# Kernel optimization log

Hardware: AMD Instinct MI355X
Metric: run time of the kernel (lower is better)

Reference implementation:

```python
import jax, jax.numpy as jnp
import numpy as np

B, D, K = 32, 400, 200
H = 8            # kernel_size (GRU hidden)
LAYERS = 4
OUT = 8


def setup_inputs() -> dict:
    key = jax.random.key(0)
    ks = jax.random.split(key, 16)
    x = jax.random.normal(ks[0], (B, D, K), dtype=jnp.float32)
    # variable-length zero padding along time per (b, k) sequence
    lengths = jax.random.randint(ks[1], (B, K), D // 2, D + 1)
    tmask = jnp.arange(D)[None, :, None] < lengths[:, None, :]   # (B, D, K)
    x = x * tmask
    s = 1.0 / np.sqrt(H)
    def u(k, shape):
        return jax.random.uniform(k, shape, jnp.float32, -s, s)
    return {
        "x": x,
        "w_ih0": u(ks[2], (2, 3 * H, 1)),
        "w_hh0": u(ks[3], (2, 3 * H, H)),
        "b_ih0": u(ks[4], (2, 3 * H)),
        "b_hh0": u(ks[5], (2, 3 * H)),
        "w_ih": u(ks[6], (LAYERS - 1, 2, 3 * H, 2 * H)),
        "w_hh": u(ks[7], (LAYERS - 1, 2, 3 * H, H)),
        "b_ih": u(ks[8], (LAYERS - 1, 2, 3 * H)),
        "b_hh": u(ks[9], (LAYERS - 1, 2, 3 * H)),
        "lin1_w": u(ks[10], (H, 2 * H)),
        "lin1_b": u(ks[11], (H,)),
        "lin2_w": u(ks[12], (OUT, H)),
        "lin2_b": u(ks[13], (OUT,)),
    }


def _gru_dir(x, mask, Wih, Whh, bih, bhh):
    # x: (N, T, in), mask: (N, T) bool -> (N, T, H); zero past each length
    gi = jnp.einsum('nti,gi->tng', x, Wih) + bih          # (T, N, 3H) input gates
    m = mask.T[:, :, None]                                 # (T, N, 1)
    h0 = jnp.zeros((x.shape[0], Whh.shape[1]), x.dtype)
    def step(h, inp):
        gi_t, m_t = inp
        gh = h @ Whh.T + bhh
        ir, iz, inn = jnp.split(gi_t, 3, axis=-1)          # PyTorch gate order r, z, n
        hr, hz, hn = jnp.split(gh, 3, axis=-1)
        r = jax.nn.sigmoid(ir + hr)
        z = jax.nn.sigmoid(iz + hz)
        n = jnp.tanh(inn + r * hn)
        h = jnp.where(m_t, (1.0 - z) * n + z * h, h)
        return h, jnp.where(m_t, h, 0.0)
    _, out = jax.lax.scan(step, h0, (gi, m))
    return out.transpose(1, 0, 2)


def _bidir_gru(x, mask, rev_idx, p):
    Wih, Whh, bih, bhh = p
    fwd = _gru_dir(x, mask, Wih[0], Whh[0], bih[0], bhh[0])
    # backward dir of a packed sequence: reverse within each valid region
    x_rev = jnp.take_along_axis(x, rev_idx[:, :, None], axis=1)
    bwd_rev = _gru_dir(x_rev, mask, Wih[1], Whh[1], bih[1], bhh[1])
    bwd = jnp.take_along_axis(bwd_rev, rev_idx[:, :, None], axis=1)
    bwd = jnp.where(mask[:, :, None], bwd, 0.0)
    return jnp.concatenate([fwd, bwd], axis=-1)


def _forward(x, w_ih0, w_hh0, b_ih0, b_hh0, w_ih, w_hh, b_ih, b_hh,
             lin1_w, lin1_b, lin2_w, lin2_b):
    b, d, k = x.shape
    seq = x.transpose(0, 2, 1).reshape(b * k, d, 1)         # (N, T, 1)
    vals = seq[:, :, 0]
    zm = vals == 0.0
    lengths = jnp.where(zm.any(axis=1), jnp.argmax(zm, axis=1), d)  # (N,)
    mask = jnp.arange(d)[None, :] < lengths[:, None]        # (N, T)
    rev_idx = jnp.clip(lengths[:, None] - 1 - jnp.arange(d)[None, :], 0, d - 1)
    h = _bidir_gru(seq, mask, rev_idx, (w_ih0, w_hh0, b_ih0, b_hh0))
    for l in range(w_ih.shape[0]):                          # layers 1..3
        h = _bidir_gru(h, mask, rev_idx, (w_ih[l], w_hh[l], b_ih[l], b_hh[l]))
    # last valid timestep per sequence (matches argmax-of-all-zero gather)
    last = jnp.take_along_axis(h, (lengths - 1)[:, None, None], axis=1)[:, 0, :]
    feat = last.reshape(b, k, -1)                           # (B, K, 2H)
    y = jax.nn.leaky_relu(feat @ lin1_w.T + lin1_b, negative_slope=0.2)
    return y @ lin2_w.T + lin2_b                            # (B, K, OUT)


def reference(x, w_ih0, w_hh0, b_ih0, b_hh0, w_ih, w_hh, b_ih, b_hh,
              lin1_w, lin1_b, lin2_w, lin2_b):
    return _forward(x, w_ih0, w_hh0, b_ih0, b_hh0, w_ih, w_hh, b_ih, b_hh,
                    lin1_w, lin1_b, lin2_w, lin2_b)
```

## Files before the change

kernel.cpp:

```cpp
#include <hip/hip_runtime.h>

#define BB 32
#define DD 400
#define KK 200
#define NN (BB*KK)
#define NBINS 512

typedef float f2 __attribute__((ext_vector_type(2)));
typedef _Float16 half_t;
typedef _Float16 f16x2 __attribute__((ext_vector_type(2)));

#if defined(__has_builtin)
#if __has_builtin(__builtin_amdgcn_fdot2)
#define HAVE_FDOT2 1
#endif
#endif

__device__ __forceinline__ float dot2(f16x2 w, f16x2 v, float acc) {
#ifdef HAVE_FDOT2
  return __builtin_amdgcn_fdot2(w, v, acc, false);
#else
  return fmaf((float)w.x, (float)v.x, fmaf((float)w.y, (float)v.y, acc));
#endif
}

__device__ __forceinline__ float fast_sigmoid(float x) {
  float e = __builtin_amdgcn_exp2f(-1.4426950408889634f * x);
  return __builtin_amdgcn_rcpf(1.0f + e);
}
__device__ __forceinline__ float fast_tanh(float x) {
  float e = __builtin_amdgcn_exp2f(-2.8853900817779268f * x);
  return 2.0f * __builtin_amdgcn_rcpf(1.0f + e) - 1.0f;
}

#define QPERM(v, P) __int_as_float(__builtin_amdgcn_mov_dpp(__float_as_int(v), (P)*0x55, 0xF, 0xF, true))
#define SWZ_XOR4(v) __int_as_float(__builtin_amdgcn_ds_swizzle(__float_as_int(v), 0x101F))

__global__ __launch_bounds__(256) void transpose_x(const float* __restrict__ x,
                                                   float* __restrict__ xt) {
  __shared__ float tile[32][33];
  int b = blockIdx.x, t0 = blockIdx.y * 32, k0 = blockIdx.z * 32;
  int tx = threadIdx.x, ty = threadIdx.y;
#pragma unroll
  for (int i = 0; i < 32; i += 8) {
    int t = t0 + ty + i, k = k0 + tx;
    tile[ty + i][tx] = (t < DD && k < KK) ? x[((size_t)b * DD + t) * KK + k] : 0.0f;
  }
  __syncthreads();
#pragma unroll
  for (int i = 0; i < 32; i += 8) {
    int k = k0 + ty + i, t = t0 + tx;
    if (k < KK && t < DD) xt[((size_t)b * KK + k) * DD + t] = tile[tx][ty + i];
  }
}

__global__ __launch_bounds__(64) void compute_lengths(const float* __restrict__ xt,
                                                      int* __restrict__ lengths,
                                                      int* __restrict__ hist) {
  int n = blockIdx.x, lane = threadIdx.x;
  int m = DD;
  for (int t = lane; t < DD; t += 64) {
    if (xt[(size_t)n * DD + t] == 0.0f) { m = t; break; }
  }
#pragma unroll
  for (int off = 1; off < 64; off <<= 1) {
    int o = __shfl_xor(m, off, 64);
    m = (o < m) ? o : m;
  }
  if (lane == 0) {
    lengths[n] = m;
    atomicAdd(&hist[m], 1);
  }
}

__global__ __launch_bounds__(64) void scan_offsets(const int* __restrict__ hist,
                                                   int* __restrict__ offs) {
  int lane = threadIdx.x;
  int v[8], tot = 0;
#pragma unroll
  for (int i = 0; i < 8; ++i) { v[i] = tot; tot += hist[lane * 8 + i]; }
  int incl = tot;
#pragma unroll
  for (int off = 1; off < 64; off <<= 1) {
    int oth = __shfl_up(incl, off, 64);
    if (lane >= off) incl += oth;
  }
  int excl = incl - tot;
#pragma unroll
  for (int i = 0; i < 8; ++i) offs[lane * 8 + i] = excl + v[i];
}

__global__ __launch_bounds__(256) void scatter_sort(const int* __restrict__ lengths,
                                                    int* __restrict__ offs,
                                                    int* __restrict__ order,
                                                    int* __restrict__ len_sorted) {
  int n = blockIdx.x * 256 + threadIdx.x;
  if (n >= NN) return;
  int len = lengths[n];
  int pos = atomicAdd(&offs[len], 1);
  order[pos] = n;
  len_sorted[pos] = len;
}

template <int IN_DIM, bool IND_IN, bool WRITE_SEQ, bool FWD_ONLY>
__global__ __launch_bounds__(256) void gru_scan(
    const void* __restrict__ in, half_t* __restrict__ out, float* __restrict__ feat,
    const int* __restrict__ len_sorted, const int* __restrict__ order,
    const float* __restrict__ Wih, const float* __restrict__ Whh,
    const float* __restrict__ bih, const float* __restrict__ bhh, int nseq) {
  int p = (blockIdx.x * 256 + threadIdx.x) >> 6;
  int lane = threadIdx.x & 63;
  int G = FWD_ONLY ? nseq : nseq * 2;
  int W = (G + 7) >> 3;
  if (p >= W) return;
  int o = (p & 1) ? (W - 1 - (p >> 1)) : (p >> 1);
  int gidx = o * 8 + (lane >> 3);
  int li = lane & 7;
  if (gidx >= G) return;
  int sg  = FWD_ONLY ? gidx : (gidx >> 1);
  int dir = FWD_ONLY ? 0 : (gidx & 1);
  int len = len_sorted[sg];

  int qb = li & 4, qbx = qb ^ 4;
  f2 wAB[3][4];
  f16x2 wi2[3][8];
  float wi1[3];
  float bs[3], bh2;
#pragma unroll
  for (int gt = 0; gt < 3; ++gt) {
    int row = dir * 24 + gt * 8 + li;
    if constexpr (IN_DIM == 16) {
#pragma unroll
      for (int q = 0; q < 8; ++q) {
        f16x2 w;
        w.x = (half_t)Wih[row * 16 + 2 * q];
        w.y = (half_t)Wih[row * 16 + 2 * q + 1];
        wi2[gt][q] = w;
      }
    } else {
      wi1[gt] = Wih[row];
    }
#pragma unroll
    for (int P = 0; P < 4; ++P) {
      f2 w; w.x = Whh[row * 8 + qb + P]; w.y = Whh[row * 8 + qbx + P];
      wAB[gt][P] = w;
    }
    bs[gt] = bih[row] + ((gt < 2) ? bhh[row] : 0.0f);
    if (gt == 2) bh2 = bhh[row];
  }

  int steps = len;
  float h = 0.0f, hx = 0.0f;

  const float* px = nullptr;
  const half_t* pxh = nullptr;
  ptrdiff_t xstep;
  if constexpr (IN_DIM == 1) {
    const float* basep = (const float*)in + (IND_IN ? (size_t)order[sg] * DD : (size_t)sg * DD);
    px = basep + ((dir == 0) ? 0 : (len - 1));
    xstep = (dir == 0) ? 1 : -1;
  } else {
    const half_t* basep = (const half_t*)in + (size_t)sg * DD * 16;
    pxh = basep + (size_t)((dir == 0) ? 0 : (len - 1)) * 16;
    xstep = (dir == 0) ? 16 : -16;
  }

  half_t* pw = nullptr; ptrdiff_t wstep = 0;
  if constexpr (WRITE_SEQ) {
    pw = out + ((size_t)sg * DD + ((dir == 0) ? 0 : (len - 1))) * 16 + dir * 8 + li;
    wstep = (dir == 0) ? 16 : -16;
  }

  auto core = [&](float a0, float a1, float a2) {
    float hq0 = QPERM(h, 0), hq1 = QPERM(h, 1), hq2 = QPERM(h, 2), hq3 = QPERM(h, 3);
    float hx0 = QPERM(hx, 0), hx1 = QPERM(hx, 1), hx2 = QPERM(hx, 2), hx3 = QPERM(hx, 3);
    f2 u0; u0.x = hq0; u0.y = hx0;
    f2 u1; u1.x = hq1; u1.y = hx1;
    f2 u2; u2.x = hq2; u2.y = hx2;
    f2 u3; u3.x = hq3; u3.y = hx3;

    f2 c0 = wAB[0][0] * u0; c0 += wAB[0][1] * u1; c0 += wAB[0][2] * u2; c0 += wAB[0][3] * u3;
    f2 c1 = wAB[1][0] * u0; c1 += wAB[1][1] * u1; c1 += wAB[1][2] * u2; c1 += wAB[1][3] * u3;
    f2 c2; c2.x = bh2; c2.y = 0.0f;
    c2 += wAB[2][0] * u0; c2 += wAB[2][1] * u1; c2 += wAB[2][2] * u2; c2 += wAB[2][3] * u3;

    float r = fast_sigmoid(a0 + c0.x + c0.y);
    float z = fast_sigmoid(a1 + c1.x + c1.y);
    float n = fast_tanh(a2 + r * (c2.x + c2.y));
    h = z * (h - n) + n;
    hx = SWZ_XOR4(h);
    if constexpr (WRITE_SEQ) { *pw = (half_t)h; pw += wstep; }
  };

  if constexpr (IN_DIM == 1) {
    float s0_, s1_, s2_, s3_;
    auto ld = [&](float& S_) { S_ = *px; px += xstep; };
    auto st = [&](float& S_, bool pf) {
      float a0 = fmaf(wi1[0], S_, bs[0]);
      float a1 = fmaf(wi1[1], S_, bs[1]);
      float a2 = fmaf(wi1[2], S_, bs[2]);
      if (pf) ld(S_);
      core(a0, a1, a2);
    };
    ld(s0_); ld(s1_); ld(s2_); ld(s3_);
    int t = 0;
    for (; t + 4 <= steps; t += 4) {
      st(s0_, true); st(s1_, true); st(s2_, true); st(s3_, true);
    }
    int rem = steps - t;
    if (rem > 0) st(s0_, false);
    if (rem > 1) st(s1_, false);
    if (rem > 2) st(s2_, false);
  } else {
    uint4 b0_[2], b1_[2], b2_[2], b3_[2];
    auto ld = [&](uint4 (&B_)[2]) {
      const uint4* q4 = reinterpret_cast<const uint4*>(pxh);
      B_[0] = q4[0]; B_[1] = q4[1];
      pxh += xstep;
    };
    auto st = [&](uint4 (&B_)[2], bool pf) {
      float a0 = bs[0], a1 = bs[1], a2 = bs[2];
#pragma unroll
      for (int q = 0; q < 2; ++q) {
        f16x2 p0 = __builtin_bit_cast(f16x2, B_[q].x);
        f16x2 p1 = __builtin_bit_cast(f16x2, B_[q].y);
        f16x2 p2 = __builtin_bit_cast(f16x2, B_[q].z);
        f16x2 p3 = __builtin_bit_cast(f16x2, B_[q].w);
        a0 = dot2(wi2[0][4*q], p0, a0); a0 = dot2(wi2[0][4*q+1], p1, a0);
        a0 = dot2(wi2[0][4*q+2], p2, a0); a0 = dot2(wi2[0][4*q+3], p3, a0);
        a1 = dot2(wi2[1][4*q], p0, a1); a1 = dot2(wi2[1][4*q+1], p1, a1);
        a1 = dot2(wi2[1][4*q+2], p2, a1); a1 = dot2(wi2[1][4*q+3], p3, a1);
        a2 = dot2(wi2[2][4*q], p0, a2); a2 = dot2(wi2[2][4*q+1], p1, a2);
        a2 = dot2(wi2[2][4*q+2], p2, a2); a2 = dot2(wi2[2][4*q+3], p3, a2);
      }
      if (pf) ld(B_);
      core(a0, a1, a2);
    };
    ld(b0_); ld(b1_); ld(b2_); ld(b3_);
    int t = 0;
    for (; t + 4 <= steps; t += 4) {
      st(b0_, true); st(b1_, true); st(b2_, true); st(b3_, true);
    }
    int rem = steps - t;
    if (rem > 0) st(b0_, false);
    if (rem > 1) st(b1_, false);
    if (rem > 2) st(b2_, false);
  }

  if constexpr (!WRITE_SEQ) {
    feat[(size_t)order[sg] * 16 + dir * 8 + li] = h;
  }
}

__global__ __launch_bounds__(256) void bwd_last(
    const half_t* __restrict__ in, float* __restrict__ feat,
    const int* __restrict__ len_sorted, const int* __restrict__ order,
    const float* __restrict__ Wih, const float* __restrict__ bih,
    const float* __restrict__ bhh, int nseq) {
  int tid = blockIdx.x * blockDim.x + threadIdx.x;
  int sg = tid >> 3, li = tid & 7;
  if (sg >= nseq) return;
  int len = len_sorted[sg];
  const half_t* xp = in + ((size_t)sg * DD + (len - 1)) * 16;
  float xv[16];
#pragma unroll
  for (int j = 0; j < 16; ++j) xv[j] = (float)xp[j];
  float a[3], bh[3];
#pragma unroll
  for (int gt = 0; gt < 3; ++gt) {
    int row = 24 + gt * 8 + li;
    const float* wp = Wih + row * 16;
    float acc = bih[row];
#pragma unroll
    for (int j = 0; j < 16; ++j) acc = fmaf(wp[j], xv[j], acc);
    a[gt] = acc;
    bh[gt] = bhh[row];
  }
  float r = fast_sigmoid(a[0] + bh[0]);
  float z = fast_sigmoid(a[1] + bh[1]);
  float n = fast_tanh(a[2] + r * bh[2]);
  float h = (1.0f - z) * n;
  feat[(size_t)order[sg] * 16 + 8 + li] = h;
}

__global__ __launch_bounds__(256) void head_kernel(
    const float* __restrict__ feat, const float* __restrict__ w1,
    const float* __restrict__ b1, const float* __restrict__ w2,
    const float* __restrict__ b2, float* __restrict__ out) {
  int n = blockIdx.x * blockDim.x + threadIdx.x;
  if (n >= NN) return;
  float f[16];
  const float4* p = reinterpret_cast<const float4*>(feat + (size_t)n * 16);
#pragma unroll
  for (int q = 0; q < 4; ++q) {
    float4 v = p[q];
    f[4*q] = v.x; f[4*q+1] = v.y; f[4*q+2] = v.z; f[4*q+3] = v.w;
  }
  float y[8];
#pragma unroll
  for (int o = 0; o < 8; ++o) {
    float s = b1[o];
#pragma unroll
    for (int j = 0; j < 16; ++j) s += f[j] * w1[o * 16 + j];
    y[o] = (s > 0.0f) ? s : 0.2f * s;
  }
#pragma unroll
  for (int o2 = 0; o2 < 8; ++o2) {
    float s = b2[o2];
#pragma unroll
    for (int o = 0; o < 8; ++o) s += y[o] * w2[o2 * 8 + o];
    out[(size_t)n * 8 + o2] = s;
  }
}

extern "C" void kernel_launch(void* const* d_in, const int* in_sizes, int n_in,
                              void* d_out, int out_size, void* d_ws, size_t ws_size,
                              hipStream_t stream) {
  const float* x      = (const float*)d_in[0];
  const float* w_ih0  = (const float*)d_in[1];
  const float* w_hh0  = (const float*)d_in[2];
  const float* b_ih0  = (const float*)d_in[3];
  const float* b_hh0  = (const float*)d_in[4];
  const float* w_ih   = (const float*)d_in[5];
  const float* w_hh   = (const float*)d_in[6];
  const float* b_ih   = (const float*)d_in[7];
  const float* b_hh   = (const float*)d_in[8];
  const float* lin1_w = (const float*)d_in[9];
  const float* lin1_b = (const float*)d_in[10];
  const float* lin2_w = (const float*)d_in[11];
  const float* lin2_b = (const float*)d_in[12];
  float* out = (float*)d_out;

  char* ws = (char*)d_ws;
  size_t off = 0;
  auto alloc = [&](size_t bytes) -> void* {
    void* p = ws + off;
    off += (bytes + 255) & ~(size_t)255;
    return p;
  };
  alloc(1024);
  float* xt         = (float*)alloc((size_t)NN * DD * sizeof(float) + 1024);
  int*   lengths    = (int*)  alloc((size_t)NN * sizeof(int));
  int*   hist       = (int*)  alloc(NBINS * sizeof(int));
  int*   offs       = (int*)  alloc(NBINS * sizeof(int));
  int*   order      = (int*)  alloc((size_t)NN * sizeof(int));
  int*   len_sorted = (int*)  alloc((size_t)NN * sizeof(int));
  float* feat       = (float*)alloc((size_t)NN * 16 * sizeof(float));
  size_t base = off;
  size_t per_seq = (size_t)DD * 16 * sizeof(half_t) * 2 + 1024;
  int Nc = NN;
  if (base + (size_t)NN * per_seq + 8192 > ws_size) {
    size_t avail = (ws_size > base + 8192) ? (ws_size - base - 8192) : 0;
    size_t nc = avail / per_seq;
    if (nc < 1) nc = 1;
    if (nc > (size_t)NN) nc = NN;
    Nc = (int)nc;
  }
  alloc(1024);
  half_t* bufA = (half_t*)alloc((size_t)Nc * DD * 16 * sizeof(half_t) + 1024);
  half_t* bufB = (half_t*)alloc((size_t)Nc * DD * 16 * sizeof(half_t) + 1024);

  hipMemsetAsync(hist, 0, NBINS * sizeof(int), stream);
  dim3 gT(BB, (DD + 31) / 32, (KK + 31) / 32), bT(32, 8, 1);
  hipLaunchKernelGGL(transpose_x, gT, bT, 0, stream, x, xt);
  hipLaunchKernelGGL(compute_lengths, dim3(NN), dim3(64), 0, stream, xt, lengths, hist);
  hipLaunchKernelGGL(scan_offsets, dim3(1), dim3(64), 0, stream, hist, offs);
  hipLaunchKernelGGL(scatter_sort, dim3((NN + 255) / 256), dim3(256), 0, stream,
                     lengths, offs, order, len_sorted);

  for (int s0 = 0; s0 < NN; s0 += Nc) {
    int ns = (NN - s0 < Nc) ? (NN - s0) : Nc;
    int W2 = (ns * 2 + 7) / 8;
    int W1 = (ns + 7) / 8;
    int blk2 = (W2 + 3) / 4;
    int blk1f = (W1 + 3) / 4;
    int blk1 = (ns * 8 + 255) / 256;
    gru_scan<1, true, true, false><<<blk2, 256, 0, stream>>>(
        (const void*)xt, bufA, nullptr, len_sorted + s0, order + s0,
        w_ih0, w_hh0, b_ih0, b_hh0, ns);
    gru_scan<16, false, true, false><<<blk2, 256, 0, stream>>>(
        (const void*)bufA, bufB, nullptr, len_sorted + s0, order + s0,
        w_ih + 0 * 2 * 24 * 16, w_hh + 0 * 2 * 24 * 8,
        b_ih + 0 * 2 * 24, b_hh + 0 * 2 * 24, ns);
    gru_scan<16, false, true, false><<<blk2, 256, 0, stream>>>(
        (const void*)bufB, bufA, nullptr, len_sorted + s0, order + s0,
        w_ih + 1 * 2 * 24 * 16, w_hh + 1 * 2 * 24 * 8,
        b_ih + 1 * 2 * 24, b_hh + 1 * 2 * 24, ns);
    gru_scan<16, false, false, true><<<blk1f, 256, 0, stream>>>(
        (const void*)bufA, nullptr, feat, len_sorted + s0, order + s0,
        w_ih + 2 * 2 * 24 * 16, w_hh + 2 * 2 * 24 * 8,
        b_ih + 2 * 2 * 24, b_hh + 2 * 2 * 24, ns);
    hipLaunchKernelGGL(bwd_last, dim3(blk1), dim3(256), 0, stream,
                       bufA, feat, len_sorted + s0, order + s0,
                       w_ih + 2 * 2 * 24 * 16, b_ih + 2 * 2 * 24, b_hh + 2 * 2 * 24, ns);
  }
  hipLaunchKernelGGL(head_kernel, dim3((NN + 255) / 256), dim3(256), 0, stream,
                     feat, lin1_w, lin1_b, lin2_w, lin2_b, out);
}
```

Baseline: 457.3 us.

## Process two length-sorted sequences per lane and split waves by direction

Each wave now advances two adjacent length-sorted sequences (A and B) in the same direction at once. The two recurrent matvecs are packed into the f2 vector lanes, so independent chains interleave and per-step latency is hidden. A wave is now assigned a single direction instead of mixing forward and backward, and per-sequence activity masks handle unequal lengths within a pair. Launch bounds request one block per SIMD-occupancy hint. The cost is higher register pressure and some wasted steps when paired lengths differ, though length sorting keeps that small.

```diff
diff --git a/kernel.cpp b/kernel.cpp
--- a/kernel.cpp
+++ b/kernel.cpp
@@ -103,152 +103,201 @@
 }
 
 template <int IN_DIM, bool IND_IN, bool WRITE_SEQ, bool FWD_ONLY>
-__global__ __launch_bounds__(256) void gru_scan(
+__global__ __launch_bounds__(256, 1) void gru_scan(
     const void* __restrict__ in, half_t* __restrict__ out, float* __restrict__ feat,
     const int* __restrict__ len_sorted, const int* __restrict__ order,
     const float* __restrict__ Wih, const float* __restrict__ Whh,
     const float* __restrict__ bih, const float* __restrict__ bhh, int nseq) {
   int p = (blockIdx.x * 256 + threadIdx.x) >> 6;
   int lane = threadIdx.x & 63;
-  int G = FWD_ONLY ? nseq : nseq * 2;
-  int W = (G + 7) >> 3;
-  if (p >= W) return;
-  int o = (p & 1) ? (W - 1 - (p >> 1)) : (p >> 1);
-  int gidx = o * 8 + (lane >> 3);
-  int li = lane & 7;
-  if (gidx >= G) return;
-  int sg  = FWD_ONLY ? gidx : (gidx >> 1);
-  int dir = FWD_ONLY ? 0 : (gidx & 1);
-  int len = len_sorted[sg];
+  int Wo = (nseq + 7) >> 3;
+  int Wp = (Wo + 1) >> 1;
+  int NW = FWD_ONLY ? Wp : 2 * Wp;
+  if (p >= NW) return;
+  int dirw = FWD_ONLY ? 0 : (p >= Wp ? 1 : 0);
+  int pl = p - dirw * Wp;
+  int q = (pl & 1) ? (Wp - 1 - (pl >> 1)) : (pl >> 1);
+  int gi8 = lane >> 3, li = lane & 7;
+  int sgA = (2 * q) * 8 + gi8;
+  int sgB = (2 * q + 1) * 8 + gi8;
+  bool vA = sgA < nseq, vB = sgB < nseq;
+  int lenA = vA ? len_sorted[sgA] : 0;
+  int lenB = vB ? len_sorted[sgB] : 0;
+  int sgAc = vA ? sgA : 0, sgBc = vB ? sgB : 0;
 
   int qb = li & 4, qbx = qb ^ 4;
-  f2 wAB[3][4];
+  f2 wAd[3][4], wBd[3][4];
   f16x2 wi2[3][8];
   float wi1[3];
   float bs[3], bh2;
 #pragma unroll
   for (int gt = 0; gt < 3; ++gt) {
-    int row = dir * 24 + gt * 8 + li;
+    int row = dirw * 24 + gt * 8 + li;
     if constexpr (IN_DIM == 16) {
 #pragma unroll
-      for (int q = 0; q < 8; ++q) {
+      for (int qq = 0; qq < 8; ++qq) {
         f16x2 w;
-        w.x = (half_t)Wih[row * 16 + 2 * q];
-        w.y = (half_t)Wih[row * 16 + 2 * q + 1];
-        wi2[gt][q] = w;
+        w.x = (half_t)Wih[row * 16 + 2 * qq];
+        w.y = (half_t)Wih[row * 16 + 2 * qq + 1];
+        wi2[gt][qq] = w;
       }
     } else {
       wi1[gt] = Wih[row];
     }
 #pragma unroll
     for (int P = 0; P < 4; ++P) {
-      f2 w; w.x = Whh[row * 8 + qb + P]; w.y = Whh[row * 8 + qbx + P];
-      wAB[gt][P] = w;
+      float wa = Whh[row * 8 + qb + P], wb = Whh[row * 8 + qbx + P];
+      f2 da; da.x = wa; da.y = wa; wAd[gt][P] = da;
+      f2 db; db.x = wb; db.y = wb; wBd[gt][P] = db;
     }
     bs[gt] = bih[row] + ((gt < 2) ? bhh[row] : 0.0f);
     if (gt == 2) bh2 = bhh[row];
   }
 
-  int steps = len;
-  float h = 0.0f, hx = 0.0f;
-
-  const float* px = nullptr;
-  const half_t* pxh = nullptr;
+  int mx = (lenA > lenB) ? lenA : lenB;
+  float hA = 0.0f, hxA = 0.0f, hB = 0.0f, hxB = 0.0f;
+
   ptrdiff_t xstep;
+  const float *pxA = nullptr, *pxB = nullptr;
+  const half_t *pxhA = nullptr, *pxhB = nullptr;
   if constexpr (IN_DIM == 1) {
-    const float* basep = (const float*)in + (IND_IN ? (size_t)order[sg] * DD : (size_t)sg * DD);
-    px = basep + ((dir == 0) ? 0 : (len - 1));
-    xstep = (dir == 0) ? 1 : -1;
+    const float* basein = (const float*)in;
+    const float* baseA = basein + (size_t)(IND_IN ? order[sgAc] : sgAc) * DD;
+    const float* baseB = basein + (size_t)(IND_IN ? order[sgBc] : sgBc) * DD;
+    pxA = baseA + ((dirw == 0) ? 0 : (lenA - 1));
+    pxB = baseB + ((dirw == 0) ? 0 : (lenB - 1));
+    xstep = (dirw == 0) ? 1 : -1;
   } else {
-    const half_t* basep = (const half_t*)in + (size_t)sg * DD * 16;
-    pxh = basep + (size_t)((dir == 0) ? 0 : (len - 1)) * 16;
-    xstep = (dir == 0) ? 16 : -16;
-  }
-
-  half_t* pw = nullptr; ptrdiff_t wstep = 0;
+    const half_t* basein = (const half_t*)in;
+    pxhA = basein + (size_t)sgAc * DD * 16 + (ptrdiff_t)((dirw == 0) ? 0 : (lenA - 1)) * 16;
+    pxhB = basein + (size_t)sgBc * DD * 16 + (ptrdiff_t)((dirw == 0) ? 0 : (lenB - 1)) * 16;
+    xstep = (dirw == 0) ? 16 : -16;
+  }
+
+  half_t *pwA = nullptr, *pwB = nullptr;
+  ptrdiff_t wstep = 0;
   if constexpr (WRITE_SEQ) {
-    pw = out + ((size_t)sg * DD + ((dir == 0) ? 0 : (len - 1))) * 16 + dir * 8 + li;
-    wstep = (dir == 0) ? 16 : -16;
-  }
-
-  auto core = [&](float a0, float a1, float a2) {
-    float hq0 = QPERM(h, 0), hq1 = QPERM(h, 1), hq2 = QPERM(h, 2), hq3 = QPERM(h, 3);
-    float hx0 = QPERM(hx, 0), hx1 = QPERM(hx, 1), hx2 = QPERM(hx, 2), hx3 = QPERM(hx, 3);
-    f2 u0; u0.x = hq0; u0.y = hx0;
-    f2 u1; u1.x = hq1; u1.y = hx1;
-    f2 u2; u2.x = hq2; u2.y = hx2;
-    f2 u3; u3.x = hq3; u3.y = hx3;
-
-    f2 c0 = wAB[0][0] * u0; c0 += wAB[0][1] * u1; c0 += wAB[0][2] * u2; c0 += wAB[0][3] * u3;
-    f2 c1 = wAB[1][0] * u0; c1 += wAB[1][1] * u1; c1 += wAB[1][2] * u2; c1 += wAB[1][3] * u3;
-    f2 c2; c2.x = bh2; c2.y = 0.0f;
-    c2 += wAB[2][0] * u0; c2 += wAB[2][1] * u1; c2 += wAB[2][2] * u2; c2 += wAB[2][3] * u3;
-
-    float r = fast_sigmoid(a0 + c0.x + c0.y);
-    float z = fast_sigmoid(a1 + c1.x + c1.y);
-    float n = fast_tanh(a2 + r * (c2.x + c2.y));
-    h = z * (h - n) + n;
-    hx = SWZ_XOR4(h);
-    if constexpr (WRITE_SEQ) { *pw = (half_t)h; pw += wstep; }
+    pwA = out + ((size_t)sgAc * DD + ((dirw == 0) ? 0 : (lenA - 1))) * 16 + dirw * 8 + li;
+    pwB = out + ((size_t)sgBc * DD + ((dirw == 0) ? 0 : (lenB - 1))) * 16 + dirw * 8 + li;
+    wstep = (dirw == 0) ? 16 : -16;
+  }
+
+  auto core2 = [&](float a0A, float a1A, float a2A,
+                   float a0B, float a1B, float a2B, bool actA, bool actB) {
+    float hqA0 = QPERM(hA, 0), hqA1 = QPERM(hA, 1), hqA2 = QPERM(hA, 2), hqA3 = QPERM(hA, 3);
+    float hxA0 = QPERM(hxA, 0), hxA1 = QPERM(hxA, 1), hxA2 = QPERM(hxA, 2), hxA3 = QPERM(hxA, 3);
+    float hqB0 = QPERM(hB, 0), hqB1 = QPERM(hB, 1), hqB2 = QPERM(hB, 2), hqB3 = QPERM(hB, 3);
+    float hxB0 = QPERM(hxB, 0), hxB1 = QPERM(hxB, 1), hxB2 = QPERM(hxB, 2), hxB3 = QPERM(hxB, 3);
+    f2 U0; U0.x = hqA0; U0.y = hqB0;
+    f2 U1; U1.x = hqA1; U1.y = hqB1;
+    f2 U2; U2.x = hqA2; U2.y = hqB2;
+    f2 U3; U3.x = hqA3; U3.y = hqB3;
+    f2 X0; X0.x = hxA0; X0.y = hxB0;
+    f2 X1; X1.x = hxA1; X1.y = hxB1;
+    f2 X2; X2.x = hxA2; X2.y = hxB2;
+    f2 X3; X3.x = hxA3; X3.y = hxB3;
+
+    f2 c0 = wAd[0][0] * U0; c0 += wAd[0][1] * U1; c0 += wAd[0][2] * U2; c0 += wAd[0][3] * U3;
+    c0 += wBd[0][0] * X0; c0 += wBd[0][1] * X1; c0 += wBd[0][2] * X2; c0 += wBd[0][3] * X3;
+    f2 c1 = wAd[1][0] * U0; c1 += wAd[1][1] * U1; c1 += wAd[1][2] * U2; c1 += wAd[1][3] * U3;
+    c1 += wBd[1][0] * X0; c1 += wBd[1][1] * X1; c1 += wBd[1][2] * X2; c1 += wBd[1][3] * X3;
+    f2 c2; c2.x = bh2; c2.y = bh2;
+    c2 += wAd[2][0] * U0; c2 += wAd[2][1] * U1; c2 += wAd[2][2] * U2; c2 += wAd[2][3] * U3;
+    c2 += wBd[2][0] * X0; c2 += wBd[2][1] * X1; c2 += wBd[2][2] * X2; c2 += wBd[2][3] * X3;
+
+    float rA = fast_sigmoid(a0A + c0.x), rB = fast_sigmoid(a0B + c0.y);
+    float zA = fast_sigmoid(a1A + c1.x), zB = fast_sigmoid(a1B + c1.y);
+    float nA = fast_tanh(a2A + rA * c2.x), nB = fast_tanh(a2B + rB * c2.y);
+    float hAn = zA * (hA - nA) + nA;
+    float hBn = zB * (hB - nB) + nB;
+    hA = actA ? hAn : hA;
+    hB = actB ? hBn : hB;
+    hxA = SWZ_XOR4(hA);
+    hxB = SWZ_XOR4(hB);
+    if constexpr (WRITE_SEQ) {
+      if (actA) *pwA = (half_t)hA;
+      if (actB) *pwB = (half_t)hB;
+      pwA += wstep; pwB += wstep;
+    }
   };
 
   if constexpr (IN_DIM == 1) {
-    float s0_, s1_, s2_, s3_;
-    auto ld = [&](float& S_) { S_ = *px; px += xstep; };
-    auto st = [&](float& S_, bool pf) {
-      float a0 = fmaf(wi1[0], S_, bs[0]);
-      float a1 = fmaf(wi1[1], S_, bs[1]);
-      float a2 = fmaf(wi1[2], S_, bs[2]);
-      if (pf) ld(S_);
-      core(a0, a1, a2);
+    float sA0_, sA1_, sA2_, sA3_, sB0_, sB1_, sB2_, sB3_;
+    auto ldA = [&](float& S_) { S_ = *pxA; pxA += xstep; };
+    auto ldB = [&](float& S_) { S_ = *pxB; pxB += xstep; };
+    auto st = [&](float& SA_, float& SB_, int t, bool pf) {
+      float a0A = fmaf(wi1[0], SA_, bs[0]);
+      float a1A = fmaf(wi1[1], SA_, bs[1]);
+      float a2A = fmaf(wi1[2], SA_, bs[2]);
+      float a0B = fmaf(wi1[0], SB_, bs[0]);
+      float a1B = fmaf(wi1[1], SB_, bs[1]);
+      float a2B = fmaf(wi1[2], SB_, bs[2]);
+      if (pf) { ldA(SA_); ldB(SB_); }
+      core2(a0A, a1A, a2A, a0B, a1B, a2B, t < lenA, t < lenB);
     };
-    ld(s0_); ld(s1_); ld(s2_); ld(s3_);
+    ldA(sA0_); ldB(sB0_); ldA(sA1_); ldB(sB1_);
+    ldA(sA2_); ldB(sB2_); ldA(sA3_); ldB(sB3_);
     int t = 0;
-    for (; t + 4 <= steps; t += 4) {
-      st(s0_, true); st(s1_, true); st(s2_, true); st(s3_, true);
+    for (; t + 4 <= mx; t += 4) {
+      st(sA0_, sB0_, t, true); st(sA1_, sB1_, t + 1, true);
+      st(sA2_, sB2_, t + 2, true); st(sA3_, sB3_, t + 3, true);
     }
-    int rem = steps - t;
-    if (rem > 0) st(s0_, false);
-    if (rem > 1) st(s1_, false);
-    if (rem > 2) st(s2_, false);
+    int rem = mx - t;
+    if (rem > 0) st(sA0_, sB0_, t, false);
+    if (rem > 1) st(sA1_, sB1_, t + 1, false);
+    if (rem > 2) st(sA2_, sB2_, t + 2, false);
   } else {
-    uint4 b0_[2], b1_[2], b2_[2], b3_[2];
-    auto ld = [&](uint4 (&B_)[2]) {
-      const uint4* q4 = reinterpret_cast<const uint4*>(pxh);
+    uint4 bA0_[2], bA1_[2], bA2_[2], bA3_[2];
+    uint4 bB0_[2], bB1_[2], bB2_[2], bB3_[2];
+    auto ldA = [&](uint4 (&B_)[2]) {
+      const uint4* q4 = reinterpret_cast<const uint4*>(pxhA);
       B_[0] = q4[0]; B_[1] = q4[1];
-      pxh += xstep;
+      pxhA += xstep;
     };
-    auto st = [&](uint4 (&B_)[2], bool pf) {
-      float a0 = bs[0], a1 = bs[1], a2 = bs[2];
-#pragma unroll
-      for (int q = 0; q < 2; ++q) {
-        f16x2 p0 = __builtin_bit_cast(f16x2, B_[q].x);
-        f16x2 p1 = __builtin_bit_cast(f16x2, B_[q].y);
-        f16x2 p2 = __builtin_bit_cast(f16x2, B_[q].z);
-        f16x2 p3 = __builtin_bit_cast(f16x2, B_[q].w);
-        a0 = dot2(wi2[0][4*q], p0, a0); a0 = dot2(wi2[0][4*q+1], p1, a0);
-        a0 = dot2(wi2[0][4*q+2], p2, a0); a0 = dot2(wi2[0][4*q+3], p3, a0);
-        a1 = dot2(wi2[1][4*q], p0, a1); a1 = dot2(wi2[1][4*q+1], p1, a1);
-        a1 = dot2(wi2[1][4*q+2], p2, a1); a1 = dot2(wi2[1][4*q+3], p3, a1);
-        a2 = dot2(wi2[2][4*q], p0, a2); a2 = dot2(wi2[2][4*q+1], p1, a2);
-        a2 = dot2(wi2[2][4*q+2], p2, a2); a2 = dot2(wi2[2][4*q+3], p3, a2);
+    auto ldB = [&](uint4 (&B_)[2]) {
+      const uint4* q4 = reinterpret_cast<const uint4*>(pxhB);
+      B_[0] = q4[0]; B_[1] = q4[1];
+      pxhB += xstep;
+    };
+    auto gi3 = [&](uint4 (&B_)[2], float& a0, float& a1, float& a2) {
+      a0 = bs[0]; a1 = bs[1]; a2 = bs[2];
+#pragma unroll
+      for (int qq = 0; qq < 2; ++qq) {
+        f16x2 p0 = __builtin_bit_cast(f16x2, B_[qq].x);
+        f16x2 p1 = __builtin_bit_cast(f16x2, B_[qq].y);
+        f16x2 p2 = __builtin_bit_cast(f16x2, B_[qq].z);
+        f16x2 p3 = __builtin_bit_cast(f16x2, B_[qq].w);
+        a0 = dot2(wi2[0][4*qq], p0, a0); a0 = dot2(wi2[0][4*qq+1], p1, a0);
+        a0 = dot2(wi2[0][4*qq+2], p2, a0); a0 = dot2(wi2[0][4*qq+3], p3, a0);
+        a1 = dot2(wi2[1][4*qq], p0, a1); a1 = dot2(wi2[1][4*qq+1], p1, a1);
+        a1 = dot2(wi2[1][4*qq+2], p2, a1); a1 = dot2(wi2[1][4*qq+3], p3, a1);
+        a2 = dot2(wi2[2][4*qq], p0, a2); a2 = dot2(wi2[2][4*qq+1], p1, a2);
+        a2 = dot2(wi2[2][4*qq+2], p2, a2); a2 = dot2(wi2[2][4*qq+3], p3, a2);
       }
-      if (pf) ld(B_);
-      core(a0, a1, a2);
     };
-    ld(b0_); ld(b1_); ld(b2_); ld(b3_);
+    auto st = [&](uint4 (&A_)[2], uint4 (&B_)[2], int t, bool pf) {
+      float a0A, a1A, a2A, a0B, a1B, a2B;
+      gi3(A_, a0A, a1A, a2A);
+      gi3(B_, a0B, a1B, a2B);
+      if (pf) { ldA(A_); ldB(B_); }
+      core2(a0A, a1A, a2A, a0B, a1B, a2B, t < lenA, t < lenB);
+    };
+    ldA(bA0_); ldB(bB0_); ldA(bA1_); ldB(bB1_);
+    ldA(bA2_); ldB(bB2_); ldA(bA3_); ldB(bB3_);
     int t = 0;
-    for (; t + 4 <= steps; t += 4) {
-      st(b0_, true); st(b1_, true); st(b2_, true); st(b3_, true);
+    for (; t + 4 <= mx; t += 4) {
+      st(bA0_, bB0_, t, true); st(bA1_, bB1_, t + 1, true);
+      st(bA2_, bB2_, t + 2, true); st(bA3_, bB3_, t + 3, true);
     }
-    int rem = steps - t;
-    if (rem > 0) st(b0_, false);
-    if (rem > 1) st(b1_, false);
-    if (rem > 2) st(b2_, false);
+    int rem = mx - t;
+    if (rem > 0) st(bA0_, bB0_, t, false);
+    if (rem > 1) st(bA1_, bB1_, t + 1, false);
+    if (rem > 2) st(bA2_, bB2_, t + 2, false);
   }
 
   if constexpr (!WRITE_SEQ) {
-    feat[(size_t)order[sg] * 16 + dir * 8 + li] = h;
+    if (vA) feat[(size_t)order[sgA] * 16 + dirw * 8 + li] = hA;
+    if (vB) feat[(size_t)order[sgB] * 16 + dirw * 8 + li] = hB;
   }
 }
 
@@ -370,10 +419,10 @@
 
   for (int s0 = 0; s0 < NN; s0 += Nc) {
     int ns = (NN - s0 < Nc) ? (NN - s0) : Nc;
-    int W2 = (ns * 2 + 7) / 8;
-    int W1 = (ns + 7) / 8;
-    int blk2 = (W2 + 3) / 4;
-    int blk1f = (W1 + 3) / 4;
+    int Wo = (ns + 7) / 8;
+    int Wp = (Wo + 1) / 2;
+    int blk2 = (2 * Wp + 3) / 4;
+    int blk1f = (Wp + 3) / 4;
     int blk1 = (ns * 8 + 255) / 256;
     gru_scan<1, true, true, false><<<blk2, 256, 0, stream>>>(
         (const void*)xt, bufA, nullptr, len_sorted + s0, order + s0,
```

Result: slower. 567.0 us (+24.0%).
